# Optimization experiments

Hardware: AMD Instinct MI355X
Metric: run time of the kernel (lower is better)

Reference implementation:

```python
import jax, jax.numpy as jnp
import numpy as np

HIDDEN = 2048
NUM_HEADS = 32
GROUP_SIZE = 4
HEAD_DIM = HIDDEN // NUM_HEADS            # 64
GROUP_NUM = NUM_HEADS // GROUP_SIZE       # 8 KV heads
B, S = 2, 2048


def setup_inputs() -> dict:
    key = jax.random.key(0)
    ks = jax.random.split(key, 7)
    sc = 1.0 / np.sqrt(HIDDEN)
    x = jax.random.normal(ks[0], (B, S, HIDDEN), dtype=jnp.float32)
    attention_mask = jnp.ones((B, S), dtype=jnp.int32)
    Wq = jax.random.normal(ks[1], (HIDDEN, HIDDEN), dtype=jnp.float32) * sc
    bq = jax.random.normal(ks[2], (HIDDEN,), dtype=jnp.float32) * 0.02
    Wk = jax.random.normal(ks[3], (HIDDEN, GROUP_NUM * HEAD_DIM), dtype=jnp.float32) * sc
    bk = jax.random.normal(ks[4], (GROUP_NUM * HEAD_DIM,), dtype=jnp.float32) * 0.02
    Wv = jax.random.normal(ks[5], (HIDDEN, GROUP_NUM * HEAD_DIM), dtype=jnp.float32) * sc
    bv = jax.random.normal(ks[6], (GROUP_NUM * HEAD_DIM,), dtype=jnp.float32) * 0.02
    return {"x": x, "attention_mask": attention_mask,
            "Wq": Wq, "bq": bq, "Wk": Wk, "bk": bk, "Wv": Wv, "bv": bv}


def reference(x, attention_mask, Wq, bq, Wk, bk, Wv, bv):
    b, s, _ = x.shape
    # projections
    q = (x @ Wq + bq).reshape(b, s, NUM_HEADS, HEAD_DIM).transpose(0, 2, 1, 3)   # (B,H,S,hd)
    k = (x @ Wk + bk).reshape(b, s, GROUP_NUM, HEAD_DIM).transpose(0, 2, 1, 3)   # (B,G,S,hd)
    v = (x @ Wv + bv).reshape(b, s, GROUP_NUM, HEAD_DIM).transpose(0, 2, 1, 3)
    # expand KV groups to full head count (head h uses group h // group_size)
    k = jnp.repeat(k, GROUP_SIZE, axis=1)                                        # (B,H,S,hd)
    v = jnp.repeat(v, GROUP_SIZE, axis=1)
    # NOTE: original torch code uses floor-division `//` for scaling and no softmax
    score = jnp.floor(jnp.einsum('bhqd,bhkd->bhqk', q, k) / np.sqrt(HEAD_DIM).astype(np.float32))
    score = jnp.where(attention_mask[:, None, None, :] == 0, -jnp.inf, score)
    out = jnp.einsum('bhqk,bhkd->bhqd', score, v)                                # (B,H,S,hd)
    return out.transpose(0, 2, 1, 3).reshape(b, s, HIDDEN)
```

## Files before the change

### kernel.cpp

```cpp
#include <hip/hip_runtime.h>
#include <math.h>

#define HIDDEN 2048
#define NHEADS 32
#define HDIM 64
#define GNUM 8
#define KVDIM 512
#define BB 2
#define SS 2048
#define MROWS (BB * SS)
#define NQKV 3072

typedef _Float16 half8 __attribute__((ext_vector_type(8)));
typedef _Float16 half4 __attribute__((ext_vector_type(4)));
typedef _Float16 half2 __attribute__((ext_vector_type(2)));
typedef __fp16 fp16x2 __attribute__((ext_vector_type(2)));
typedef float floatx4 __attribute__((ext_vector_type(4)));

#define MFMA16(a, b, c) __builtin_amdgcn_mfma_f32_16x16x32_f16((a), (b), (c), 0, 0, 0)

__device__ __forceinline__ void split_f32(float x, _Float16& hi, _Float16& lo) {
    hi = (_Float16)x;
    lo = (_Float16)((x - (float)hi) * 2048.0f);
}

__device__ __forceinline__ void load_lds16(const void* g, void* l) {
    __builtin_amdgcn_global_load_lds(
        (const __attribute__((address_space(1))) void*)g,
        (__attribute__((address_space(3))) void*)l, 16, 0, 0);
}

__device__ __forceinline__ void permswap32(unsigned& a, unsigned& b) {
    asm volatile("v_permlane32_swap_b32 %0, %1" : "+v"(a), "+v"(b));
}
__device__ __forceinline__ void permswap16(unsigned& a, unsigned& b) {
    asm volatile("v_permlane16_swap_b32 %0, %1" : "+v"(a), "+v"(b));
}

__device__ __forceinline__ unsigned pk_f16(float a, float b) {
    union { fp16x2 h; unsigned u; } c;
    c.h = __builtin_amdgcn_cvt_pkrtz(a, b);
    return c.u;
}

__global__ __launch_bounds__(256)
void split_x(const float* __restrict__ x, _Float16* __restrict__ xh,
             _Float16* __restrict__ xl, int n4) {
    for (int idx = blockIdx.x * 256 + threadIdx.x; idx < n4; idx += gridDim.x * 256) {
        floatx4 v = reinterpret_cast<const floatx4*>(x)[idx];
        half4 h, l;
        #pragma unroll
        for (int e = 0; e < 4; ++e) { _Float16 hi, lo; split_f32(v[e], hi, lo); h[e] = hi; l[e] = lo; }
        reinterpret_cast<half4*>(xh)[idx] = h;
        reinterpret_cast<half4*>(xl)[idx] = l;
    }
}

__global__ __launch_bounds__(256)
void split_wt(const float* __restrict__ W, int N, int n0,
              _Float16* __restrict__ Wth, _Float16* __restrict__ Wtl) {
    __shared__ float tile[64][68];
    const int tid = threadIdx.x;
    const int kb = blockIdx.x, nb = blockIdx.y;
    #pragma unroll
    for (int i = 0; i < 4; ++i) {
        int idx = tid + i * 256;
        int r = idx >> 4, c4 = idx & 15;
        floatx4 v = *reinterpret_cast<const floatx4*>(&W[(size_t)(kb * 64 + r) * N + nb * 64 + c4 * 4]);
        *reinterpret_cast<floatx4*>(&tile[r][c4 * 4]) = v;
    }
    __syncthreads();
    #pragma unroll
    for (int i = 0; i < 4; ++i) {
        int idx = tid + i * 256;
        int r2 = idx >> 4, c2 = (idx & 15) * 4;
        half4 h, l;
        #pragma unroll
        for (int e = 0; e < 4; ++e) {
            _Float16 hi, lo;
            split_f32(tile[c2 + e][r2], hi, lo);
            h[e] = hi; l[e] = lo;
        }
        size_t o = (size_t)(n0 + nb * 64 + r2) * HIDDEN + kb * 64 + c2;
        *reinterpret_cast<half4*>(&Wth[o]) = h;
        *reinterpret_cast<half4*>(&Wtl[o]) = l;
    }
}

__global__ __launch_bounds__(256)
void biascat_k(const float* __restrict__ bq, const float* __restrict__ bk,
               const float* __restrict__ bv, float* __restrict__ bias) {
    int i = blockIdx.x * 256 + threadIdx.x;
    if (i < 2048) bias[i] = bq[i];
    else if (i < 2560) bias[i] = bk[i - 2048];
    else if (i < NQKV) bias[i] = bv[i - 2560];
}

__global__ __launch_bounds__(256, 2)
void gemm_qkv(const _Float16* __restrict__ xh, const _Float16* __restrict__ xl,
              const _Float16* __restrict__ Wth, const _Float16* __restrict__ Wtl,
              const float* __restrict__ bias,
              _Float16* __restrict__ qh, _Float16* __restrict__ ql,
              _Float16* __restrict__ khs, _Float16* __restrict__ kls,
              _Float16* __restrict__ vh) {
    __shared__ __align__(16) _Float16 Ah[128 * 64];
    __shared__ __align__(16) _Float16 Al[128 * 64];
    __shared__ __align__(16) _Float16 Bh[128 * 64];
    __shared__ __align__(16) _Float16 Bl[128 * 64];

    const int tid  = threadIdx.x;
    const int lane = tid & 63;
    const int w    = tid >> 6;
    const int wm   = w >> 1, wn = w & 1;
    const int bm   = blockIdx.x, bn = blockIdx.y;
    const int ml   = lane & 15;
    const int kg8  = (lane >> 4) * 8;
    const bool lo3 = (bn < 20);

    const _Float16* gsrc;
    _Float16* ldst;
    if      (w == 0) { gsrc = xh  + (size_t)(bm * 128) * HIDDEN; ldst = Ah; }
    else if (w == 1) { gsrc = xl  + (size_t)(bm * 128) * HIDDEN; ldst = Al; }
    else if (w == 2) { gsrc = Wth + (size_t)(bn * 128) * HIDDEN; ldst = Bh; }
    else             { gsrc = Wtl + (size_t)(bn * 128) * HIDDEN; ldst = Bl; }
    const bool do_stage = lo3 || (w == 0) || (w == 2);

    floatx4 acc0[4][4] = {};
    floatx4 accL[4][4] = {};

    for (int k0 = 0; k0 < HIDDEN; k0 += 64) {
        if (do_stage) {
            #pragma unroll
            for (int i = 0; i < 16; ++i) {
                int L   = i * 1024 + lane * 16;
                int row = L >> 7;
                int off = (L & 127) ^ ((row & 7) << 4);
                const void* gp = (const char*)(gsrc + (size_t)row * HIDDEN + k0) + off;
                void* lp = (char*)ldst + i * 1024;
                load_lds16(gp, lp);
            }
        }
        __syncthreads();

        #pragma unroll
        for (int kc = 0; kc < 2; ++kc) {
            half8 a_h[4], b_h[4];
            #pragma unroll
            for (int r = 0; r < 4; ++r) {
                int row = wm * 64 + r * 16 + ml;
                int byt = row * 128 + (((kc * 64 + kg8 * 2)) ^ ((row & 7) << 4));
                a_h[r] = *reinterpret_cast<const half8*>((const char*)Ah + byt);
            }
            #pragma unroll
            for (int c = 0; c < 4; ++c) {
                int row = wn * 64 + c * 16 + ml;
                int byt = row * 128 + (((kc * 64 + kg8 * 2)) ^ ((row & 7) << 4));
                b_h[c] = *reinterpret_cast<const half8*>((const char*)Bh + byt);
            }
            if (lo3) {
                half8 a_l[4], b_l[4];
                #pragma unroll
                for (int r = 0; r < 4; ++r) {
                    int row = wm * 64 + r * 16 + ml;
                    int byt = row * 128 + (((kc * 64 + kg8 * 2)) ^ ((row & 7) << 4));
                    a_l[r] = *reinterpret_cast<const half8*>((const char*)Al + byt);
                }
                #pragma unroll
                for (int c = 0; c < 4; ++c) {
                    int row = wn * 64 + c * 16 + ml;
                    int byt = row * 128 + (((kc * 64 + kg8 * 2)) ^ ((row & 7) << 4));
                    b_l[c] = *reinterpret_cast<const half8*>((const char*)Bl + byt);
                }
                #pragma unroll
                for (int r = 0; r < 4; ++r)
                    #pragma unroll
                    for (int c = 0; c < 4; ++c) {
                        acc0[r][c] = MFMA16(a_h[r], b_h[c], acc0[r][c]);
                        accL[r][c] = MFMA16(a_h[r], b_l[c], accL[r][c]);
                        accL[r][c] = MFMA16(a_l[r], b_h[c], accL[r][c]);
                    }
            } else {
                #pragma unroll
                for (int r = 0; r < 4; ++r)
                    #pragma unroll
                    for (int c = 0; c < 4; ++c)
                        acc0[r][c] = MFMA16(a_h[r], b_h[c], acc0[r][c]);
            }
        }
        __syncthreads();
    }

    #pragma unroll
    for (int c = 0; c < 4; ++c) {
        int colg = bn * 128 + wn * 64 + c * 16 + ml;
        float bval = bias[colg];
        #pragma unroll
        for (int r = 0; r < 4; ++r) {
            int rowg = bm * 128 + wm * 64 + r * 16 + (lane >> 4) * 4;
            #pragma unroll
            for (int reg = 0; reg < 4; ++reg) {
                float val = acc0[r][c][reg] + accL[r][c][reg] * (1.0f / 2048.0f) + bval;
                int rr = rowg + reg;
                if (colg < 2048) {
                    _Float16 hi, lo; split_f32(val, hi, lo);
                    qh[(size_t)rr * HIDDEN + colg] = hi;
                    ql[(size_t)rr * HIDDEN + colg] = lo;
                } else if (colg < 2560) {
                    int ck = colg - 2048;
                    int gk = ck >> 6, dk = ck & 63;
                    int bk_ = rr >> 11, sk_ = rr & 2047;
                    int kk = sk_ & 63;
                    size_t baseK = ((size_t)((bk_ * 8 + gk) * 32 + (sk_ >> 6))) * 4096
                                 + kk * 64 + (dk ^ ((kk & 7) << 3));
                    _Float16 hi, lo; split_f32(val, hi, lo);
                    khs[baseK] = hi;
                    kls[baseK] = lo;
                } else {
                    vh[(size_t)rr * KVDIM + (colg - 2560)] = (_Float16)val;
                }
            }
        }
    }
}

__global__ __launch_bounds__(256, 2)
void attn5(const _Float16* __restrict__ qh, const _Float16* __restrict__ ql,
           const _Float16* __restrict__ khs, const _Float16* __restrict__ kls,
           const _Float16* __restrict__ vh, const int* __restrict__ mask,
           float* __restrict__ out) {
    __shared__ __align__(16) _Float16 Ksh[64 * 64];
    __shared__ __align__(16) _Float16 Ksl[64 * 64];
    __shared__ __align__(16) _Float16 Vst[64][72];

    const int tid  = threadIdx.x;
    const int lane = tid & 63;
    const int w    = tid >> 6;
    const int ml   = lane & 15;
    const int lg   = lane >> 4;
    const int kg8  = lg * 8;

    const int f_  = blockIdx.y * 32 + blockIdx.x;
    const int bg  = (f_ & 7) | ((f_ >> 8) << 3);
    const int qt  = (f_ >> 3) & 31;
    const int b   = bg >> 3, g = bg & 7;

    half8 qhf[4][2], qlf[4][2];
    {
        size_t rowbase = (size_t)(b * SS + qt * 64 + w * 16 + ml) * HIDDEN;
        #pragma unroll
        for (int hh = 0; hh < 4; ++hh) {
            int hcol = (g * 4 + hh) * HDIM;
            #pragma unroll
            for (int gch = 0; gch < 2; ++gch) {
                half8 a = *reinterpret_cast<const half8*>(&qh[rowbase + hcol + gch * 32 + kg8]);
                half8 c = *reinterpret_cast<const half8*>(&ql[rowbase + hcol + gch * 32 + kg8]);
                qhf[hh][gch] = a * (_Float16)0.125f;
                qlf[hh][gch] = c * (_Float16)0.125f;
            }
        }
    }

    const _Float16* ktile_h = khs + (size_t)(bg * 32) * 4096;
    const _Float16* ktile_l = kls + (size_t)(bg * 32) * 4096;
    const _Float16* vbg = vh + (size_t)b * SS * KVDIM + g * HDIM;
    const int* mb = mask + b * SS;

    floatx4 oacc[4][4] = {};

    for (int kt = 0; kt < SS / 64; ++kt) {
        __syncthreads();
        if (w == 0) {
            #pragma unroll
            for (int j = 0; j < 8; ++j)
                load_lds16((const char*)(ktile_h + (size_t)kt * 4096) + j * 1024 + lane * 16,
                           (char*)Ksh + j * 1024);
        } else if (w == 1) {
            #pragma unroll
            for (int j = 0; j < 8; ++j)
                load_lds16((const char*)(ktile_l + (size_t)kt * 4096) + j * 1024 + lane * 16,
                           (char*)Ksl + j * 1024);
        }
        {
            int rp = (tid & 31) * 2, c8 = (tid >> 5) * 8;
            half8 v0 = *reinterpret_cast<const half8*>(&vbg[(size_t)(kt * 64 + rp) * KVDIM + c8]);
            half8 v1 = *reinterpret_cast<const half8*>(&vbg[(size_t)(kt * 64 + rp + 1) * KVDIM + c8]);
            #pragma unroll
            for (int e = 0; e < 8; ++e)
                *reinterpret_cast<half2*>(&Vst[c8 + e][rp]) = half2{v0[e], v1[e]};
        }
        __syncthreads();

        half8 av[4][2];
        #pragma unroll
        for (int f = 0; f < 4; ++f)
            #pragma unroll
            for (int kc = 0; kc < 2; ++kc)
                av[f][kc] = *reinterpret_cast<const half8*>(&Vst[f * 16 + ml][kc * 32 + kg8]);

        int4 m4v[4];
        #pragma unroll
        for (int fc = 0; fc < 4; ++fc)
            m4v[fc] = *reinterpret_cast<const int4*>(&mb[kt * 64 + fc * 16 + lg * 4]);

        __builtin_amdgcn_s_setprio(1);

        unsigned h2[4][4][2];
        #pragma unroll
        for (int fc = 0; fc < 4; ++fc) {
            int krow = fc * 16 + ml;
            int xo = (krow & 7) << 3;
            half8 k_h[2], k_l[2];
            #pragma unroll
            for (int gch = 0; gch < 2; ++gch) {
                k_h[gch] = *reinterpret_cast<const half8*>(&Ksh[krow * 64 + ((gch * 32 + kg8) ^ xo)]);
                k_l[gch] = *reinterpret_cast<const half8*>(&Ksl[krow * 64 + ((gch * 32 + kg8) ^ xo)]);
            }
            #pragma unroll
            for (int hh = 0; hh < 4; ++hh) {
                floatx4 s0 = {}, sl = {};
                s0 = MFMA16(k_h[0], qhf[hh][0], s0);
                s0 = MFMA16(k_h[1], qhf[hh][1], s0);
                sl = MFMA16(k_l[0], qhf[hh][0], sl);
                sl = MFMA16(k_l[1], qhf[hh][1], sl);
                sl = MFMA16(k_h[0], qlf[hh][0], sl);
                sl = MFMA16(k_h[1], qlf[hh][1], sl);
                float sv[4];
                #pragma unroll
                for (int r = 0; r < 4; ++r) {
                    float t = floorf(fmaf(sl[r], 1.0f / 2048.0f, s0[r]));
                    sv[r] = (m4v[fc][r] == 0) ? -INFINITY : t;
                }
                h2[hh][fc][0] = pk_f16(sv[0], sv[1]);
                h2[hh][fc][1] = pk_f16(sv[2], sv[3]);
            }
        }

        #pragma unroll
        for (int hh = 0; hh < 4; ++hh) {
            #pragma unroll
            for (int kc = 0; kc < 2; ++kc) {
                unsigned t0 = h2[hh][2 * kc][0], tA = h2[hh][2 * kc + 1][0];
                unsigned t1 = h2[hh][2 * kc][1], tB = h2[hh][2 * kc + 1][1];
                permswap32(t0, tA); permswap16(t0, tA);
                permswap32(t1, tB); permswap16(t1, tB);
                union { unsigned u[4]; half8 h; } bu;
                bu.u[0] = t0; bu.u[1] = t1; bu.u[2] = tA; bu.u[3] = tB;
                #pragma unroll
                for (int f = 0; f < 4; ++f)
                    oacc[hh][f] = MFMA16(av[f][kc], bu.h, oacc[hh][f]);
            }
        }
        __builtin_amdgcn_s_setprio(0);
    }

    #pragma unroll
    for (int hh = 0; hh < 4; ++hh) {
        int hcol = (g * 4 + hh) * HDIM;
        #pragma unroll
        for (int f = 0; f < 4; ++f) {
            size_t row = (size_t)(b * SS + qt * 64 + w * 16 + ml);
            *reinterpret_cast<floatx4*>(&out[row * HIDDEN + hcol + f * 16 + lg * 4]) = oacc[hh][f];
        }
    }
}

extern "C" void kernel_launch(void* const* d_in, const int* in_sizes, int n_in,
                              void* d_out, int out_size, void* d_ws, size_t ws_size,
                              hipStream_t stream) {
    (void)in_sizes; (void)n_in; (void)out_size; (void)ws_size;
    const float* x    = (const float*)d_in[0];
    const int*   mask = (const int*)d_in[1];
    const float* Wq   = (const float*)d_in[2];
    const float* bq   = (const float*)d_in[3];
    const float* Wk   = (const float*)d_in[4];
    const float* bk   = (const float*)d_in[5];
    const float* Wv   = (const float*)d_in[6];
    const float* bv   = (const float*)d_in[7];

    _Float16* ws16 = (_Float16*)d_ws;
    size_t o = 0;
    auto alloc16 = [&](size_t n) { _Float16* p = ws16 + o; o += n; return p; };
    _Float16* xh  = alloc16((size_t)MROWS * HIDDEN);
    _Float16* xl  = alloc16((size_t)MROWS * HIDDEN);
    _Float16* Wth = alloc16((size_t)NQKV * HIDDEN);
    _Float16* Wtl = alloc16((size_t)NQKV * HIDDEN);
    _Float16* qh  = alloc16((size_t)MROWS * HIDDEN);
    _Float16* ql  = alloc16((size_t)MROWS * HIDDEN);
    _Float16* khs = alloc16((size_t)MROWS * KVDIM);
    _Float16* kls = alloc16((size_t)MROWS * KVDIM);
    _Float16* vh  = alloc16((size_t)MROWS * KVDIM);
    float* biascat = (float*)(ws16 + o);

    split_x<<<2048, 256, 0, stream>>>(x, xh, xl, MROWS * HIDDEN / 4);
    split_wt<<<dim3(32, 32), 256, 0, stream>>>(Wq, HIDDEN, 0,    Wth, Wtl);
    split_wt<<<dim3(32, 8),  256, 0, stream>>>(Wk, KVDIM, 2048, Wth, Wtl);
    split_wt<<<dim3(32, 8),  256, 0, stream>>>(Wv, KVDIM, 2560, Wth, Wtl);
    biascat_k<<<12, 256, 0, stream>>>(bq, bk, bv, biascat);
    gemm_qkv<<<dim3(MROWS / 128, NQKV / 128), 256, 0, stream>>>(
        xh, xl, Wth, Wtl, biascat, qh, ql, khs, kls, vh);
    attn5<<<dim3(32, 16), 256, 0, stream>>>(qh, ql, khs, kls, vh, mask, (float*)d_out);
}
```

Before: 305.5 us.

## Pre-transpose and swizzle V tiles in QKV GEMM epilogue for direct LDS loads

The QKV GEMM epilogue now writes V pre-transposed into per-(batch,group) 64x64 tiles with an XOR swizzle, matching the K layout. The attention kernel then fills LDS with one wave's direct global-to-LDS loads instead of every thread doing a register-level transpose with half2 scattered stores. This removes per-iteration transpose work and the padded LDS array. The cost is scattered 2-byte stores in the GEMM epilogue for V, and the V load now rests on a single wave.

New measurement: 298.8 us. 1.02x faster.

```diff
diff --git a/kernel.cpp b/kernel.cpp
--- a/kernel.cpp
+++ b/kernel.cpp
@@ -102,7 +102,7 @@
               const float* __restrict__ bias,
               _Float16* __restrict__ qh, _Float16* __restrict__ ql,
               _Float16* __restrict__ khs, _Float16* __restrict__ kls,
-              _Float16* __restrict__ vh) {
+              _Float16* __restrict__ vhs) {
     __shared__ __align__(16) _Float16 Ah[128 * 64];
     __shared__ __align__(16) _Float16 Al[128 * 64];
     __shared__ __align__(16) _Float16 Bh[128 * 64];
@@ -216,7 +216,13 @@
                     khs[baseK] = hi;
                     kls[baseK] = lo;
                 } else {
-                    vh[(size_t)rr * KVDIM + (colg - 2560)] = (_Float16)val;
+                    int ck = colg - 2560;
+                    int gk = ck >> 6, dk = ck & 63;
+                    int bk_ = rr >> 11, sk_ = rr & 2047;
+                    int s6 = sk_ & 63;
+                    size_t baseV = ((size_t)((bk_ * 8 + gk) * 32 + (sk_ >> 6))) * 4096
+                                 + dk * 64 + (s6 ^ ((dk & 7) << 3));
+                    vhs[baseV] = (_Float16)val;
                 }
             }
         }
@@ -224,13 +230,13 @@
 }
 
 __global__ __launch_bounds__(256, 2)
-void attn5(const _Float16* __restrict__ qh, const _Float16* __restrict__ ql,
+void attn7(const _Float16* __restrict__ qh, const _Float16* __restrict__ ql,
            const _Float16* __restrict__ khs, const _Float16* __restrict__ kls,
-           const _Float16* __restrict__ vh, const int* __restrict__ mask,
+           const _Float16* __restrict__ vhs, const int* __restrict__ mask,
            float* __restrict__ out) {
     __shared__ __align__(16) _Float16 Ksh[64 * 64];
     __shared__ __align__(16) _Float16 Ksl[64 * 64];
-    __shared__ __align__(16) _Float16 Vst[64][72];
+    __shared__ __align__(16) _Float16 Vs[64 * 64];
 
     const int tid  = threadIdx.x;
     const int lane = tid & 63;
@@ -262,7 +268,7 @@
 
     const _Float16* ktile_h = khs + (size_t)(bg * 32) * 4096;
     const _Float16* ktile_l = kls + (size_t)(bg * 32) * 4096;
-    const _Float16* vbg = vh + (size_t)b * SS * KVDIM + g * HDIM;
+    const _Float16* vtile   = vhs + (size_t)(bg * 32) * 4096;
     const int* mb = mask + b * SS;
 
     floatx4 oacc[4][4] = {};
@@ -279,23 +285,24 @@
             for (int j = 0; j < 8; ++j)
                 load_lds16((const char*)(ktile_l + (size_t)kt * 4096) + j * 1024 + lane * 16,
                            (char*)Ksl + j * 1024);
-        }
-        {
-            int rp = (tid & 31) * 2, c8 = (tid >> 5) * 8;
-            half8 v0 = *reinterpret_cast<const half8*>(&vbg[(size_t)(kt * 64 + rp) * KVDIM + c8]);
-            half8 v1 = *reinterpret_cast<const half8*>(&vbg[(size_t)(kt * 64 + rp + 1) * KVDIM + c8]);
-            #pragma unroll
-            for (int e = 0; e < 8; ++e)
-                *reinterpret_cast<half2*>(&Vst[c8 + e][rp]) = half2{v0[e], v1[e]};
+        } else if (w == 2) {
+            #pragma unroll
+            for (int j = 0; j < 8; ++j)
+                load_lds16((const char*)(vtile + (size_t)kt * 4096) + j * 1024 + lane * 16,
+                           (char*)Vs + j * 1024);
         }
         __syncthreads();
 
         half8 av[4][2];
         #pragma unroll
-        for (int f = 0; f < 4; ++f)
+        for (int f = 0; f < 4; ++f) {
+            int vrow = f * 16 + ml;
+            int vxo = (vrow & 7) << 3;
             #pragma unroll
             for (int kc = 0; kc < 2; ++kc)
-                av[f][kc] = *reinterpret_cast<const half8*>(&Vst[f * 16 + ml][kc * 32 + kg8]);
+                av[f][kc] = *reinterpret_cast<const half8*>(
+                    &Vs[vrow * 64 + ((kc * 32 + kg8) ^ vxo)]);
+        }
 
         int4 m4v[4];
         #pragma unroll
@@ -388,7 +395,7 @@
     _Float16* ql  = alloc16((size_t)MROWS * HIDDEN);
     _Float16* khs = alloc16((size_t)MROWS * KVDIM);
     _Float16* kls = alloc16((size_t)MROWS * KVDIM);
-    _Float16* vh  = alloc16((size_t)MROWS * KVDIM);
+    _Float16* vhs = alloc16((size_t)MROWS * KVDIM);
     float* biascat = (float*)(ws16 + o);
 
     split_x<<<2048, 256, 0, stream>>>(x, xh, xl, MROWS * HIDDEN / 4);
@@ -397,6 +404,6 @@
     split_wt<<<dim3(32, 8),  256, 0, stream>>>(Wv, KVDIM, 2560, Wth, Wtl);
     biascat_k<<<12, 256, 0, stream>>>(bq, bk, bv, biascat);
     gemm_qkv<<<dim3(MROWS / 128, NQKV / 128), 256, 0, stream>>>(
-        xh, xl, Wth, Wtl, biascat, qh, ql, khs, kls, vh);
-    attn5<<<dim3(32, 16), 256, 0, stream>>>(qh, ql, khs, kls, vh, mask, (float*)d_out);
-}
+        xh, xl, Wth, Wtl, biascat, qh, ql, khs, kls, vhs);
+    attn7<<<dim3(32, 16), 256, 0, stream>>>(qh, ql, khs, kls, vhs, mask, (float*)d_out);
+}
```
